# Optimization experiments

Hardware: AMD Instinct MI355X
Metric: run time of the kernel (lower is better)

The kernel has to match this reference:

```python
import jax, jax.numpy as jnp
import numpy as np

NUM_NODES = 1_000_000
IN_F, HID_F, OUT_F = 128, 128, 128
N0, N1, T = 16384, 4096, 16


def _safediv(a, b):
    return a / jnp.where(b == 0, jnp.ones_like(b), b)


def _conv(h, nodeset, nb_nodes, nb_w, Qw, Qb, Ww, Wb):
    # gather self + neighbor embeddings (irregular access)
    h_self = h[nodeset]                                   # [n, in]
    h_nb = h[nb_nodes]                                    # [n, T, in]
    q = jax.nn.leaky_relu(jnp.einsum('nti,hi->nth', h_nb, Qw) + Qb)
    agg = _safediv((nb_w[:, :, None] * q).sum(1), nb_w.sum(1, keepdims=True))  # [n, hid]
    h_cat = jnp.concatenate([h_self, agg], axis=1)        # [n, in+hid]
    h_new = jax.nn.leaky_relu(h_cat @ Ww.T + Wb)          # [n, out]
    nrm = jnp.linalg.norm(h_new, axis=1, keepdims=True)
    return _safediv(h_new, nrm)


def setup_inputs() -> dict:
    key = jax.random.key(0)
    ks = jax.random.split(key, 16)
    xav = lambda k, o, i: jax.random.uniform(k, (o, i), jnp.float32, -1.0, 1.0) * jnp.sqrt(6.0 / (o + i)) * jnp.sqrt(2.0)
    return {
        'h': jax.random.normal(ks[0], (NUM_NODES, IN_F), jnp.float32),
        'Qw0': xav(ks[1], HID_F, IN_F), 'Qb0': jnp.zeros((HID_F,), jnp.float32),
        'Ww0': xav(ks[2], HID_F, IN_F + HID_F), 'Wb0': jnp.zeros((HID_F,), jnp.float32),
        'Qw1': xav(ks[3], OUT_F, HID_F), 'Qb1': jnp.zeros((OUT_F,), jnp.float32),
        'Ww1': xav(ks[4], OUT_F, HID_F + OUT_F), 'Wb1': jnp.zeros((OUT_F,), jnp.float32),
        'nodeset0': jax.random.randint(ks[5], (N0,), 0, NUM_NODES, jnp.int32),
        'nb_nodes0': jax.random.randint(ks[6], (N0, T), 0, NUM_NODES, jnp.int32),
        'nb_weights0': jax.random.uniform(ks[7], (N0, T), jnp.float32),
        'nodeset1': jax.random.randint(ks[8], (N1,), 0, NUM_NODES, jnp.int32),
        'nb_nodes1': jax.random.randint(ks[9], (N1, T), 0, NUM_NODES, jnp.int32),
        'nb_weights1': jax.random.uniform(ks[10], (N1, T), jnp.float32),
    }


def reference(h, Qw0, Qb0, Ww0, Wb0, Qw1, Qb1, Ww1, Wb1,
              nodeset0, nb_nodes0, nb_weights0,
              nodeset1, nb_nodes1, nb_weights1):
    # layer 0: conv then scatter back into embedding table
    new0 = _conv(h, nodeset0, nb_nodes0, nb_weights0, Qw0, Qb0, Ww0, Wb0)
    h = h.at[nodeset0].set(new0)
    # layer 1
    new1 = _conv(h, nodeset1, nb_nodes1, nb_weights1, Qw1, Qb1, Ww1, Wb1)
    h = h.at[nodeset1].set(new1)
    return h[nodeset1]  # [N1, OUT_F]
```

## Files before the change

### kernel.cpp

```cpp
#include <hip/hip_runtime.h>
#include <hip/hip_bf16.h>
#include <math.h>

#define NN 1000000
#define F 128
#define N0 16384
#define N1 4096
#define HS0 65536
#define HS1 16384

typedef __attribute__((ext_vector_type(8))) short bf16x8;
typedef __attribute__((ext_vector_type(4))) float f32x4;

__device__ inline unsigned short f2b(float f) {
    union { float f; unsigned u; } v; v.f = f;
    unsigned r = v.u + 0x7FFFu + ((v.u >> 16) & 1u);
    return (unsigned short)(r >> 16);
}

__device__ inline bf16x8 pack8(float4 a, float4 b) {
    union { __hip_bfloat162 h2[4]; bf16x8 v; } u;
    u.h2[0] = __float22bfloat162_rn(make_float2(a.x, a.y));
    u.h2[1] = __float22bfloat162_rn(make_float2(a.z, a.w));
    u.h2[2] = __float22bfloat162_rn(make_float2(b.x, b.y));
    u.h2[3] = __float22bfloat162_rn(make_float2(b.z, b.w));
    return u.v;
}


__device__ inline void hins(unsigned* __restrict__ keys, unsigned* __restrict__ vals,
                            unsigned mask, unsigned g, unsigned pos1) {
    unsigned s = (g * 2654435761u) & mask;
    while (true) {
        unsigned prev = atomicCAS(&keys[s], 0xFFFFFFFFu, g);
        if (prev == 0xFFFFFFFFu || prev == g) { atomicMax(&vals[s], pos1); return; }
        s = (s + 1) & mask;
    }
}

__device__ inline int hfind(const unsigned* __restrict__ keys,
                            const unsigned* __restrict__ vals,
                            unsigned mask, unsigned g) {
    unsigned s = (g * 2654435761u) & mask;
    while (true) {
        unsigned k = keys[s];
        if (k == g) return (int)vals[s] - 1;
        if (k == 0xFFFFFFFFu) return -1;
        s = (s + 1) & mask;
    }
}


__global__ void k_pre(unsigned* __restrict__ k0, unsigned* __restrict__ v0,
                      unsigned* __restrict__ k1, unsigned* __restrict__ v1,
                      const float* __restrict__ Qw0, const float* __restrict__ Qw1,
                      const float* __restrict__ Ww0, const float* __restrict__ Ww1,
                      unsigned short* __restrict__ Qw0b, unsigned short* __restrict__ Qw1b,
                      unsigned short* __restrict__ Ww0b, unsigned short* __restrict__ Ww1b) {
    int i = blockIdx.x * blockDim.x + threadIdx.x;
    int nt = gridDim.x * blockDim.x;
    for (int j = i; j < HS0; j += nt) { k0[j] = 0xFFFFFFFFu; v0[j] = 0u; }
    for (int j = i; j < HS1; j += nt) { k1[j] = 0xFFFFFFFFu; v1[j] = 0u; }
    for (int j = i; j < 128 * 128; j += nt) { Qw0b[j] = f2b(Qw0[j]); Qw1b[j] = f2b(Qw1[j]); }
    for (int j = i; j < 128 * 256; j += nt) { Ww0b[j] = f2b(Ww0[j]); Ww1b[j] = f2b(Ww1[j]); }
}


__global__ __launch_bounds__(512, 4) void k_layer(
    const float* __restrict__ h, const unsigned short* __restrict__ newprevb,
    const unsigned* __restrict__ lk, const unsigned* __restrict__ lv, unsigned lmask,
    const int* __restrict__ nodeset, const int* __restrict__ nb,
    const float* __restrict__ nbw,
    const unsigned short* __restrict__ Qwb, const float* __restrict__ Qb,
    const unsigned short* __restrict__ Wwb, const float* __restrict__ Wb,
    float* __restrict__ outf, unsigned short* __restrict__ outb,
    const int* __restrict__ ins0, unsigned* __restrict__ ik0, unsigned* __restrict__ iv0,
    const int* __restrict__ ins1, unsigned* __restrict__ ik1, unsigned* __restrict__ iv1)
{
    __shared__ unsigned short lQ[128 * 128];
    __shared__ unsigned short lA[16 * 256];
    __shared__ float sred[8][16];
    const int tid = threadIdx.x;
    const int wid = tid >> 6, lane = tid & 63;
    const int row = lane & 15, kg = lane >> 4;
    const long mbase = (long)blockIdx.x * 16;

    if (ik0) {
        int base = blockIdx.x * 16;
        if (tid < 16) {
            int i = base + tid;
            if (i < N0) hins(ik0, iv0, HS0 - 1, (unsigned)ins0[i], (unsigned)(i + 1));
        } else if (tid < 32) {
            int i = base + tid - 16;
            if (i < N1) hins(ik1, iv1, HS1 - 1, (unsigned)ins1[i], (unsigned)(i + 1));
        }
    }

    const int sr = tid >> 4, sq = tid & 15;
    const bool sact = tid < 256;
    bool sredir = false;
    float4 sv0, sv1;
    uint4 sb;
    if (sact) {
        int gs = nodeset[mbase + sr];
        int p = lk ? hfind(lk, lv, lmask, (unsigned)gs) : -1;
        if (p >= 0) {
            sredir = true;
            sb = *(const uint4*)(newprevb + (size_t)p * F + sq * 8);
        } else {
            const float4* s = (const float4*)(h + (size_t)gs * F) + sq * 2;
            sv0 = s[0]; sv1 = s[1];
        }
    }

    const long nodebase = mbase + wid * 2;
    int g0 = nb[nodebase * 16 + row];
    int g1 = nb[(nodebase + 1) * 16 + row];
    int p0 = lk ? hfind(lk, lv, lmask, (unsigned)g0) : -1;
    int p1 = lk ? hfind(lk, lv, lmask, (unsigned)g1) : -1;
    bf16x8 Ab[2][4];
    float4 av[2][8];
    if (p0 >= 0) {
        const bf16x8* s = (const bf16x8*)(newprevb + (size_t)p0 * F);
#pragma unroll
        for (int kk = 0; kk < 4; ++kk) Ab[0][kk] = s[kk * 4 + kg];
    } else {
        const float4* s4 = (const float4*)(h + (size_t)g0 * F);
#pragma unroll
        for (int kk = 0; kk < 4; ++kk) {
            av[0][kk * 2]     = s4[kk * 8 + kg * 2];
            av[0][kk * 2 + 1] = s4[kk * 8 + kg * 2 + 1];
        }
    }
    if (p1 >= 0) {
        const bf16x8* s = (const bf16x8*)(newprevb + (size_t)p1 * F);
#pragma unroll
        for (int kk = 0; kk < 4; ++kk) Ab[1][kk] = s[kk * 4 + kg];
    } else {
        const float4* s4 = (const float4*)(h + (size_t)g1 * F);
#pragma unroll
        for (int kk = 0; kk < 4; ++kk) {
            av[1][kk * 2]     = s4[kk * 8 + kg * 2];
            av[1][kk * 2 + 1] = s4[kk * 8 + kg * 2 + 1];
        }
    }

    for (int c = tid; c < 2048; c += 512) {
        int j = c >> 4;
        uint4 v = ((const uint4*)Qwb)[c];
        *(uint4*)((char*)lQ + ((c << 4) ^ ((j & 7) << 4))) = v;
    }

    float w[2][4];
#pragma unroll
    for (int nn = 0; nn < 2; ++nn)
#pragma unroll
        for (int r = 0; r < 4; ++r) w[nn][r] = nbw[(nodebase + nn) * 16 + kg * 4 + r];

    if (p0 < 0) {
#pragma unroll
        for (int kk = 0; kk < 4; ++kk) Ab[0][kk] = pack8(av[0][kk * 2], av[0][kk * 2 + 1]);
    }
    if (p1 < 0) {
#pragma unroll
        for (int kk = 0; kk < 4; ++kk) Ab[1][kk] = pack8(av[1][kk * 2], av[1][kk * 2 + 1]);
    }

    if (sact) {
        int b0 = sr * 512 + sq * 16;
        int swz = (sr & 7) << 4;
        if (sredir) *(uint4*)((char*)lA + (b0 ^ swz)) = sb;
        else        *(bf16x8*)((char*)lA + (b0 ^ swz)) = pack8(sv0, sv1);
    }
    __syncthreads();

    float inv[2];
#pragma unroll
    for (int nn = 0; nn < 2; ++nn) {
        float ws = w[nn][0] + w[nn][1] + w[nn][2] + w[nn][3];
        ws += __shfl_xor(ws, 16);
        ws += __shfl_xor(ws, 32);
        inv[nn] = (ws == 0.f) ? 1.f : 1.f / ws;
    }

#pragma unroll 1
    for (int half = 0; half < 2; ++half) {
        f32x4 acc[2][4];
#pragma unroll
        for (int nn = 0; nn < 2; ++nn)
#pragma unroll
            for (int jt = 0; jt < 4; ++jt)
                acc[nn][jt] = (f32x4){0.f, 0.f, 0.f, 0.f};

#pragma unroll
        for (int kk = 0; kk < 4; ++kk) {
            bf16x8 Bf[4];
#pragma unroll
            for (int jt = 0; jt < 4; ++jt) {
                int j = (half * 4 + jt) * 16 + row;
                int byte = ((j << 8) + (kk << 6) + (kg << 4)) ^ ((j & 7) << 4);
                Bf[jt] = *(bf16x8*)((char*)lQ + byte);
            }
#pragma unroll
            for (int jt = 0; jt < 4; ++jt) {
                acc[0][jt] = __builtin_amdgcn_mfma_f32_16x16x32_bf16(Ab[0][kk], Bf[jt], acc[0][jt], 0, 0, 0);
                acc[1][jt] = __builtin_amdgcn_mfma_f32_16x16x32_bf16(Ab[1][kk], Bf[jt], acc[1][jt], 0, 0, 0);
            }
        }

#pragma unroll
        for (int nn = 0; nn < 2; ++nn) {
            int nl = wid * 2 + nn;
#pragma unroll
            for (int jt = 0; jt < 4; ++jt) {
                int jtg = half * 4 + jt;
                float qb = Qb[jtg * 16 + row];
                float t = 0.f;
#pragma unroll
                for (int r = 0; r < 4; ++r) {
                    float v = acc[nn][jt][r] + qb;
                    v = v > 0.f ? v : 0.01f * v;
                    t = fmaf(w[nn][r], v, t);
                }
                t += __shfl_xor(t, 16);
                t += __shfl_xor(t, 32);
                if (lane < 16) {
                    int byte = (nl * 512 + 256 + jtg * 32 + lane * 2) ^ ((nl & 7) << 4);
                    *(unsigned short*)((char*)lA + byte) = f2b(t * inv[nn]);
                }
            }
        }
    }
    __syncthreads();

    const int j = wid * 16 + row;
    f32x4 dacc = (f32x4){0.f, 0.f, 0.f, 0.f};
#pragma unroll
    for (int kk = 0; kk < 8; ++kk) {
        bf16x8 a = *(bf16x8*)((char*)lA + ((row * 512 + kk * 64 + kg * 16) ^ ((row & 7) << 4)));
        bf16x8 b = ((const bf16x8*)(Wwb + (size_t)j * 256))[kk * 4 + kg];
        dacc = __builtin_amdgcn_mfma_f32_16x16x32_bf16(a, b, dacc, 0, 0, 0);
    }

    float wb = Wb[j];
    float ss[4];
#pragma unroll
    for (int r = 0; r < 4; ++r) {
        float v = dacc[r] + wb;
        v = v > 0.f ? v : 0.01f * v;
        dacc[r] = v;
        ss[r] = v * v;
    }
#pragma unroll
    for (int r = 0; r < 4; ++r) {
        ss[r] += __shfl_xor(ss[r], 1);
        ss[r] += __shfl_xor(ss[r], 2);
        ss[r] += __shfl_xor(ss[r], 4);
        ss[r] += __shfl_xor(ss[r], 8);
    }
    if (row == 0) {
#pragma unroll
        for (int r = 0; r < 4; ++r) sred[wid][kg * 4 + r] = ss[r];
    }
    __syncthreads();
    float invn[4];
#pragma unroll
    for (int r = 0; r < 4; ++r) {
        float s = 0.f;
#pragma unroll
        for (int w8 = 0; w8 < 8; ++w8) s += sred[w8][kg * 4 + r];
        float n = sqrtf(s);
        invn[r] = (n == 0.f) ? 1.f : 1.f / n;
    }
    if (outf) {
#pragma unroll
        for (int r = 0; r < 4; ++r)
            outf[(size_t)(mbase + kg * 4 + r) * F + j] = dacc[r] * invn[r];
    } else {
#pragma unroll
        for (int r = 0; r < 4; ++r)
            outb[(size_t)(mbase + kg * 4 + r) * F + j] = f2b(dacc[r] * invn[r]);
    }
}


__global__ void k_fix(const unsigned* __restrict__ k1, const unsigned* __restrict__ v1,
                      const int* __restrict__ ns1, float* __restrict__ out, int n) {
    int i = blockIdx.x * blockDim.x + threadIdx.x;
    if (i < n) {
        int p = hfind(k1, v1, HS1 - 1, (unsigned)ns1[i]);
        if (p != i) {
            float4* o = (float4*)out;
#pragma unroll
            for (int c = 0; c < 32; ++c) o[(size_t)i * 32 + c] = o[(size_t)p * 32 + c];
        }
    }
}


extern "C" void kernel_launch(void* const* d_in, const int* in_sizes, int n_in,
                              void* d_out, int out_size, void* d_ws, size_t ws_size,
                              hipStream_t stream) {
    const float* h    = (const float*)d_in[0];
    const float* Qw0  = (const float*)d_in[1];
    const float* Qb0  = (const float*)d_in[2];
    const float* Ww0  = (const float*)d_in[3];
    const float* Wb0  = (const float*)d_in[4];
    const float* Qw1  = (const float*)d_in[5];
    const float* Qb1  = (const float*)d_in[6];
    const float* Ww1  = (const float*)d_in[7];
    const float* Wb1  = (const float*)d_in[8];
    const int*   ns0  = (const int*)d_in[9];
    const int*   nb0  = (const int*)d_in[10];
    const float* nbw0 = (const float*)d_in[11];
    const int*   ns1  = (const int*)d_in[12];
    const int*   nb1  = (const int*)d_in[13];
    const float* nbw1 = (const float*)d_in[14];

    unsigned* hk0 = (unsigned*)d_ws;
    unsigned* hv0 = hk0 + HS0;
    unsigned* hk1 = hv0 + HS0;
    unsigned* hv1 = hk1 + HS1;
    unsigned short* new0b = (unsigned short*)(hv1 + HS1);
    unsigned short* Qw0b = new0b + (size_t)N0 * F;
    unsigned short* Qw1b = Qw0b + 128 * 128;
    unsigned short* Ww0b = Qw1b + 128 * 128;
    unsigned short* Ww1b = Ww0b + 128 * 256;

    k_pre<<<128, 256, 0, stream>>>(hk0, hv0, hk1, hv1,
                                   Qw0, Qw1, Ww0, Ww1, Qw0b, Qw1b, Ww0b, Ww1b);

    k_layer<<<N0 / 16, 512, 0, stream>>>(h, nullptr, nullptr, nullptr, 0u,
                                         ns0, nb0, nbw0, Qw0b, Qb0, Ww0b, Wb0,
                                         nullptr, new0b,
                                         ns0, hk0, hv0, ns1, hk1, hv1);

    k_layer<<<N1 / 16, 512, 0, stream>>>(h, new0b, hk0, hv0, HS0 - 1,
                                         ns1, nb1, nbw1, Qw1b, Qb1, Ww1b, Wb1,
                                         (float*)d_out, nullptr,
                                         nullptr, nullptr, nullptr, nullptr, nullptr, nullptr);

    k_fix<<<(N1 + 255) / 256, 256, 0, stream>>>(hk1, hv1, ns1, (float*)d_out, N1);
}
```

Baseline: 79.18 us.

## Permute K dimension so neighbor row gathers become lane-contiguous coalesced float4 loads

Reorders the K (feature) index of the Q and W weight matrices during preprocessing with a permutation, and matches that permutation in the bf16 intermediate outputs and the self-feature LDS writes. With this layout each lane group reads float4 elements c*4+kg, so the four kg lanes read adjacent 16-byte chunks instead of strided pairs. The goal is better coalescing of the irregular neighbor-row gathers from the large h table. In exchange it adds index arithmetic and splits the self-feature LDS store into two 8-byte writes. Correctness depends on every producer and consumer of the bf16 intermediate using the same permutation.

```diff
diff --git a/kernel.cpp b/kernel.cpp
--- a/kernel.cpp
+++ b/kernel.cpp
@@ -25,6 +25,18 @@
     u.h2[2] = __float22bfloat162_rn(make_float2(b.x, b.y));
     u.h2[3] = __float22bfloat162_rn(make_float2(b.z, b.w));
     return u.v;
+}
+
+__device__ inline uint2 pack4(float4 a) {
+    union { __hip_bfloat162 h2[2]; uint2 v; } u;
+    u.h2[0] = __float22bfloat162_rn(make_float2(a.x, a.y));
+    u.h2[1] = __float22bfloat162_rn(make_float2(a.z, a.w));
+    return u.v;
+}
+
+__device__ inline int kperm(int p) {
+    int kk = p >> 5, kg = (p >> 3) & 3, e = p & 7;
+    return kk * 32 + kg * 4 + (e < 4 ? e : e + 12);
 }
 
 
@@ -61,8 +73,16 @@
     int nt = gridDim.x * blockDim.x;
     for (int j = i; j < HS0; j += nt) { k0[j] = 0xFFFFFFFFu; v0[j] = 0u; }
     for (int j = i; j < HS1; j += nt) { k1[j] = 0xFFFFFFFFu; v1[j] = 0u; }
-    for (int j = i; j < 128 * 128; j += nt) { Qw0b[j] = f2b(Qw0[j]); Qw1b[j] = f2b(Qw1[j]); }
-    for (int j = i; j < 128 * 256; j += nt) { Ww0b[j] = f2b(Ww0[j]); Ww1b[j] = f2b(Ww1[j]); }
+    for (int j = i; j < 128 * 128; j += nt) {
+        int r = j >> 7, p = j & 127;
+        int src = (r << 7) + kperm(p);
+        Qw0b[j] = f2b(Qw0[src]); Qw1b[j] = f2b(Qw1[src]);
+    }
+    for (int j = i; j < 128 * 256; j += nt) {
+        int r = j >> 8, p = j & 255;
+        int src = (r << 8) + (p < 128 ? kperm(p) : p);
+        Ww0b[j] = f2b(Ww0[src]); Ww1b[j] = f2b(Ww1[src]);
+    }
 }
 
 
@@ -108,8 +128,8 @@
             sredir = true;
             sb = *(const uint4*)(newprevb + (size_t)p * F + sq * 8);
         } else {
-            const float4* s = (const float4*)(h + (size_t)gs * F) + sq * 2;
-            sv0 = s[0]; sv1 = s[1];
+            const float4* s = (const float4*)(h + (size_t)gs * F);
+            sv0 = s[sq]; sv1 = s[sq + 16];
         }
     }
 
@@ -127,10 +147,7 @@
     } else {
         const float4* s4 = (const float4*)(h + (size_t)g0 * F);
 #pragma unroll
-        for (int kk = 0; kk < 4; ++kk) {
-            av[0][kk * 2]     = s4[kk * 8 + kg * 2];
-            av[0][kk * 2 + 1] = s4[kk * 8 + kg * 2 + 1];
-        }
+        for (int c = 0; c < 8; ++c) av[0][c] = s4[c * 4 + kg];
     }
     if (p1 >= 0) {
         const bf16x8* s = (const bf16x8*)(newprevb + (size_t)p1 * F);
@@ -139,10 +156,7 @@
     } else {
         const float4* s4 = (const float4*)(h + (size_t)g1 * F);
 #pragma unroll
-        for (int kk = 0; kk < 4; ++kk) {
-            av[1][kk * 2]     = s4[kk * 8 + kg * 2];
-            av[1][kk * 2 + 1] = s4[kk * 8 + kg * 2 + 1];
-        }
+        for (int c = 0; c < 8; ++c) av[1][c] = s4[c * 4 + kg];
     }
 
     for (int c = tid; c < 2048; c += 512) {
@@ -159,18 +173,24 @@
 
     if (p0 < 0) {
 #pragma unroll
-        for (int kk = 0; kk < 4; ++kk) Ab[0][kk] = pack8(av[0][kk * 2], av[0][kk * 2 + 1]);
+        for (int kk = 0; kk < 4; ++kk) Ab[0][kk] = pack8(av[0][2 * kk], av[0][2 * kk + 1]);
     }
     if (p1 < 0) {
 #pragma unroll
-        for (int kk = 0; kk < 4; ++kk) Ab[1][kk] = pack8(av[1][kk * 2], av[1][kk * 2 + 1]);
+        for (int kk = 0; kk < 4; ++kk) Ab[1][kk] = pack8(av[1][2 * kk], av[1][2 * kk + 1]);
     }
 
     if (sact) {
-        int b0 = sr * 512 + sq * 16;
         int swz = (sr & 7) << 4;
-        if (sredir) *(uint4*)((char*)lA + (b0 ^ swz)) = sb;
-        else        *(bf16x8*)((char*)lA + (b0 ^ swz)) = pack8(sv0, sv1);
+        if (sredir) {
+            int b0 = sr * 512 + sq * 16;
+            *(uint4*)((char*)lA + (b0 ^ swz)) = sb;
+        } else {
+            int pp = ((sq >> 3) << 5) + ((sq & 3) << 3) + ((sq & 4) ? 4 : 0);
+            int b1 = sr * 512 + pp * 2;
+            *(uint2*)((char*)lA + (b1 ^ swz)) = pack4(sv0);
+            *(uint2*)((char*)lA + ((b1 + 128) ^ swz)) = pack4(sv1);
+        }
     }
     __syncthreads();
 
@@ -277,9 +297,10 @@
         for (int r = 0; r < 4; ++r)
             outf[(size_t)(mbase + kg * 4 + r) * F + j] = dacc[r] * invn[r];
     } else {
+        int pj = ((j >> 5) << 5) + (((j & 15) >> 2) << 3) + ((j & 16) ? 4 : 0) + (j & 3);
 #pragma unroll
         for (int r = 0; r < 4; ++r)
-            outb[(size_t)(mbase + kg * 4 + r) * F + j] = f2b(dacc[r] * invn[r]);
+            outb[(size_t)(mbase + kg * 4 + r) * F + pj] = f2b(dacc[r] * invn[r]);
     }
 }
 
```

After: 79.55 us. Within noise of the previous version (+0.5%).
